# Performance work log

Measured on AMD Instinct MI355X. Metric: run time of the kernel, lower is better.

## Reference

```python
import jax, jax.numpy as jnp
import numpy as np

B, T, D, E, C = 2, 2048, 2048, 8, 512
O1 = D // E  # per-expert hidden width (out_features // num_experts)


def setup_inputs() -> dict:
    key = jax.random.key(0)
    k = jax.random.split(key, 8)
    s = 1.0 / np.sqrt(D)
    return {
        "x": jax.random.normal(k[0], (B, T, D), dtype=jnp.float32),
        "dispatch_mask": jax.random.uniform(k[1], (B, T, E, C), dtype=jnp.float32),
        "combine_array": jax.random.uniform(k[2], (B, T, E, C), dtype=jnp.float32),
        # contract weights: nn.Linear(D, D) reshaped to (E, D//E, D)
        "W1": jax.random.uniform(k[3], (E, O1, D), jnp.float32, -s, s),
        "b1": jax.random.uniform(k[4], (E, O1), jnp.float32, -s, s),
        # expand weights: nn.Linear(D, D) reshaped to (E, D, D//E)
        "W2": jax.random.uniform(k[5], (E, D, O1), jnp.float32, -s, s),
        "b2": jax.random.uniform(k[6], (D,), jnp.float32, -s, s),
    }


def reference(x, dispatch_mask, combine_array, W1, b1, W2, b2):
    # --- ExpertsChooseMaskedContract ---
    # einsum('btd,btec,eod->beco') split into two GEMM-shaped contractions
    xe = jnp.einsum('btd,btec->becd', x, dispatch_mask)          # [B,E,C,D]
    h = jnp.einsum('becd,eod->beco', xe, W1) + b1[None, :, None, :]  # [B,E,C,O1]
    # --- GELU (torch nn.GELU default = exact erf form) ---
    h = jax.nn.gelu(h, approximate=False)
    # --- ExpertsChooseMaskedExpand (homogeneous-coords bias == add b2 then combine) ---
    y = jnp.einsum('beci,eoi->beco', h, W2) + b2[None, None, None, :]  # [B,E,C,D]
    out = jnp.einsum('beco,btec->bto', y, combine_array)          # [B,T,D]
    return out
```

## Files before the change

### kernel.cpp

```cpp
#include <hip/hip_runtime.h>
#include <math.h>

#define BB 2
#define TT 2048
#define DD 2048
#define EE 8
#define CCv 512
#define OO1 256

typedef unsigned short u16;
typedef __bf16 bf16x8 __attribute__((ext_vector_type(8)));
typedef float f32x4 __attribute__((ext_vector_type(4)));

__device__ __forceinline__ u16 f2bf(float f) {
    unsigned u = __float_as_uint(f);
    unsigned r = (u + 0x7fffu + ((u >> 16) & 1u)) >> 16;
    return (u16)r;
}

__device__ __forceinline__ void gload16(const void* g, void* s) {
    __builtin_amdgcn_global_load_lds(
        (const __attribute__((address_space(1))) void*)g,
        (__attribute__((address_space(3))) void*)s, 16, 0, 0);
}

__global__ __launch_bounds__(256) void conv_cast(const float* __restrict__ in,
                                                 u16* __restrict__ out, long n) {
    long i = ((long)blockIdx.x * 256 + threadIdx.x) * 4;
    float4 v = *(const float4*)&in[i];
    ushort4 o; o.x = f2bf(v.x); o.y = f2bf(v.y); o.z = f2bf(v.z); o.w = f2bf(v.w);
    *(ushort4*)&out[i] = o;
}

__global__ __launch_bounds__(256) void dup_cast(const float* __restrict__ in,
                                                u16* __restrict__ out, long dup) {
    long i = ((long)blockIdx.x * 256 + threadIdx.x) * 4;
    float4 v = *(const float4*)&in[i];
    ushort4 o; o.x = f2bf(v.x); o.y = f2bf(v.y); o.z = f2bf(v.z); o.w = f2bf(v.w);
    *(ushort4*)&out[i] = o;
    *(ushort4*)&out[i + dup] = o;
}

__global__ __launch_bounds__(256) void gelu_fuse(const float* __restrict__ P,
                                                 const float* __restrict__ b1,
                                                 u16* __restrict__ h) {
    long i = ((long)blockIdx.x * 256 + threadIdx.x) * 4;
    const int o = (int)(i & 255);
    const int e = (int)((i >> 17) & 7);
    float4 a = *(const float4*)&P[i];
    float4 b = *(const float4*)&P[i + 4194304];
    float4 bb = *(const float4*)&b1[e * 256 + o];
    float r0 = a.x + b.x + bb.x, r1 = a.y + b.y + bb.y;
    float r2 = a.z + b.z + bb.z, r3 = a.w + b.w + bb.w;
    ushort4 o4;
    o4.x = f2bf(0.5f * r0 * (1.0f + erff(r0 * 0.70710678118654752f)));
    o4.y = f2bf(0.5f * r1 * (1.0f + erff(r1 * 0.70710678118654752f)));
    o4.z = f2bf(0.5f * r2 * (1.0f + erff(r2 * 0.70710678118654752f)));
    o4.w = f2bf(0.5f * r3 * (1.0f + erff(r3 * 0.70710678118654752f)));
    *(ushort4*)&h[i] = o4;
}

__global__ __launch_bounds__(256) void transpose_conv(
    const float* __restrict__ in, long inHi, long inLo, int modZ, long sIn,
    u16* __restrict__ out, long outZ, long sOut)
{
    __shared__ float tile[32][33];
    const int z = blockIdx.z;
    const float* ib = in + (long)(z / modZ) * inHi + (long)(z % modZ) * inLo;
    u16* ob = out + (long)z * outZ;
    const int t0 = blockIdx.y * 32, c0 = blockIdx.x * 32;
    const int tid = threadIdx.x;
    const int r = tid >> 3, c4 = (tid & 7) * 4;

    float4 v = *(const float4*)&ib[(long)(t0 + r) * sIn + c0 + c4];
    tile[r][c4 + 0] = v.x; tile[r][c4 + 1] = v.y;
    tile[r][c4 + 2] = v.z; tile[r][c4 + 3] = v.w;
    __syncthreads();

    const int oc = tid >> 3, t4 = (tid & 7) * 4;
    ushort4 o;
    o.x = f2bf(tile[t4 + 0][oc]);
    o.y = f2bf(tile[t4 + 1][oc]);
    o.z = f2bf(tile[t4 + 2][oc]);
    o.w = f2bf(tile[t4 + 3][oc]);
    *(ushort4*)&ob[(long)(c0 + oc) * sOut + t0 + t4] = o;
}

template<int EPI, int OUTBF>
__global__ __launch_bounds__(256)
void mfma_gemm(const u16* __restrict__ A, long ldA, long aHi, long aLo, int modA,
               const u16* __restrict__ B, long ldB, long bHi, long bLo, int modB,
               void* __restrict__ Cout, long ldC, long cHi, long cLo, int modC,
               const float* __restrict__ bias, long biasLo, int modBias,
               int M, int N, int K)
{
    __shared__ __align__(16) char smem[32768];
    char* smA = smem;
    char* smB = smem + 16384;

    const int z = blockIdx.z;
    const char* Ab = (const char*)(A + (long)(z / modA) * aHi + (long)(z % modA) * aLo);
    const char* Bb = (const char*)(B + (long)(z / modB) * bHi + (long)(z % modB) * bLo);
    const long ldAb = ldA * 2, ldBb = ldB * 2;

    const int m0 = blockIdx.y * 128, n0 = blockIdx.x * 128;
    const int tid = threadIdx.x;
    const int l = tid & 63;
    const int w = tid >> 6;
    const int wm = w >> 1, wn = w & 1;

    const int srow = l >> 3;
    const int schunk = (l & 7) ^ srow;
    const int frow = l & 15;
    const int fgrp = l >> 4;
    const int fch0 = fgrp ^ (l & 7);

    int aoff[4], boff[4];
#pragma unroll
    for (int i = 0; i < 4; ++i) {
        aoff[i] = (wm * 64 + i * 16 + frow) * 128 + fch0 * 16;
        boff[i] = (wn * 64 + i * 16 + frow) * 128 + fch0 * 16;
    }

    f32x4 acc[4][4];
    const f32x4 zero4 = {0.f, 0.f, 0.f, 0.f};
#pragma unroll
    for (int i = 0; i < 4; ++i)
#pragma unroll
        for (int j = 0; j < 4; ++j) acc[i][j] = zero4;

    const long sgo = (long)schunk * 16;

    for (int k0 = 0; k0 < K; k0 += 64) {
        const long kb = (long)k0 * 2;
#pragma unroll
        for (int j = 0; j < 4; ++j) {
            const int rr = (j * 4 + w) * 8 + srow;
            gload16(Ab + (long)(m0 + rr) * ldAb + kb + sgo, smA + (j * 4 + w) * 1024);
            gload16(Bb + (long)(n0 + rr) * ldBb + kb + sgo, smB + (j * 4 + w) * 1024);
        }
        __syncthreads();
#pragma unroll
        for (int kk = 0; kk < 2; ++kk) {
            const int kx = kk * 64;
            bf16x8 af[4], bfr[4];
#pragma unroll
            for (int i = 0; i < 4; ++i) af[i] = *(const bf16x8*)(smA + (aoff[i] ^ kx));
#pragma unroll
            for (int i = 0; i < 4; ++i) bfr[i] = *(const bf16x8*)(smB + (boff[i] ^ kx));
#pragma unroll
            for (int mi = 0; mi < 4; ++mi)
#pragma unroll
                for (int ni = 0; ni < 4; ++ni)
                    acc[mi][ni] = __builtin_amdgcn_mfma_f32_16x16x32_bf16(
                        af[mi], bfr[ni], acc[mi][ni], 0, 0, 0);
        }
        __syncthreads();
    }

    const long cbase = (long)(z / modC) * cHi + (long)(z % modC) * cLo;
    const float* biasB = (EPI != 0) ? (bias + (long)(z % modBias) * biasLo) : nullptr;
#pragma unroll
    for (int mi = 0; mi < 4; ++mi) {
#pragma unroll
        for (int ni = 0; ni < 4; ++ni) {
            const int col = n0 + wn * 64 + ni * 16 + frow;
            const int rowb = m0 + wm * 64 + mi * 16 + fgrp * 4;
#pragma unroll
            for (int r = 0; r < 4; ++r) {
                float v = acc[mi][ni][r];
                const int row = rowb + r;
                if (EPI == 3) v += biasB[row];
                const long idx = cbase + (long)row * ldC + col;
                if (OUTBF) ((u16*)Cout)[idx] = f2bf(v);
                else       ((float*)Cout)[idx] = v;
            }
        }
    }
}

template<int OUTBF>
__global__ __launch_bounds__(512, 2)
void mfma_gemm_256(const u16* __restrict__ A, long ldA, long aHi, long aLo, int modA,
                   const u16* __restrict__ B, long ldB, long bHi, long bLo, int modB,
                   void* __restrict__ Cout, long ldC, long cHi, long cLo, int modC,
                   int M, int N, int K)
{
    __shared__ __align__(16) char smem[131072];

    const int z = blockIdx.z;
    const char* Ab = (const char*)(A + (long)(z / modA) * aHi + (long)(z % modA) * aLo);
    const char* Bb = (const char*)(B + (long)(z / modB) * bHi + (long)(z % modB) * bLo);
    const long ldAb = ldA * 2, ldBb = ldB * 2;

    const int m0 = blockIdx.y * 256, n0 = blockIdx.x * 256;
    const int tid = threadIdx.x;
    const int l = tid & 63;
    const int w = tid >> 6;
    const int wm = w >> 2, wn = w & 3;

    const int srow = l >> 3;
    const int schunk = (l & 7) ^ srow;
    const long sgo = (long)schunk * 16;
    const int frow = l & 15, fgrp = l >> 4;
    const int cs0 = (fgrp ^ (l & 7)) * 16;

    auto stage = [&](int kt, int bsel, int half, int j) {
        const int rr = (w * 2 + j) * 8 + srow;
        const char* gb = (half < 2) ? Ab : Bb;
        const long ld = (half < 2) ? ldAb : ldBb;
        const int gr = ((half < 2) ? m0 + half * 128 : n0 + (half - 2) * 128) + rr;
        gload16(gb + (long)gr * ld + (long)kt * 128 + sgo,
                smem + bsel * 65536 + half * 16384 + (w * 2 + j) * 1024);
    };

    f32x4 acc[2][4][2][2];
    const f32x4 zero4 = {0.f, 0.f, 0.f, 0.f};
#pragma unroll
    for (int qm = 0; qm < 2; ++qm)
#pragma unroll
        for (int mi = 0; mi < 4; ++mi)
#pragma unroll
            for (int qn = 0; qn < 2; ++qn)
#pragma unroll
                for (int ni = 0; ni < 2; ++ni) acc[qm][mi][qn][ni] = zero4;

    int aoff[4], boff[2];
#pragma unroll
    for (int mi = 0; mi < 4; ++mi) aoff[mi] = (wm * 64 + mi * 16 + frow) * 128 + cs0;
#pragma unroll
    for (int ni = 0; ni < 2; ++ni) boff[ni] = (wn * 32 + ni * 16 + frow) * 128 + cs0;

    stage(0, 0, 0, 0); stage(0, 0, 0, 1);
    stage(0, 0, 2, 0); stage(0, 0, 2, 1);
    stage(0, 0, 3, 0); stage(0, 0, 3, 1);
    stage(0, 0, 1, 0); stage(0, 0, 1, 1);
    asm volatile("s_waitcnt vmcnt(4)" ::: "memory");
    __builtin_amdgcn_s_barrier();

    const int NT = K >> 6;
    for (int kt = 0; kt < NT; ++kt) {
        const char* buf = smem + (kt & 1) * 65536;
        const int sb = (kt & 1) ^ 1;
        const bool pf = (kt + 1) < NT;
        const int kn = kt + 1;
        bf16x8 af[4][2], bq0[2][2], bq1[2][2];

#pragma unroll
        for (int mi = 0; mi < 4; ++mi) {
            af[mi][0] = *(const bf16x8*)(buf + aoff[mi]);
            af[mi][1] = *(const bf16x8*)(buf + (aoff[mi] ^ 64));
        }
#pragma unroll
        for (int ni = 0; ni < 2; ++ni) {
            bq0[ni][0] = *(const bf16x8*)(buf + 32768 + boff[ni]);
            bq0[ni][1] = *(const bf16x8*)(buf + 32768 + (boff[ni] ^ 64));
        }
        if (pf) { stage(kn, sb, 0, 0); stage(kn, sb, 0, 1); }
        if (pf) { asm volatile("s_waitcnt vmcnt(4)" ::: "memory"); }
        else    { asm volatile("s_waitcnt vmcnt(2)" ::: "memory"); }
        __builtin_amdgcn_s_barrier();
        __builtin_amdgcn_s_setprio(1);
#pragma unroll
        for (int kk = 0; kk < 2; ++kk)
#pragma unroll
            for (int mi = 0; mi < 4; ++mi)
#pragma unroll
                for (int ni = 0; ni < 2; ++ni)
                    acc[0][mi][0][ni] = __builtin_amdgcn_mfma_f32_16x16x32_bf16(
                        af[mi][kk], bq0[ni][kk], acc[0][mi][0][ni], 0, 0, 0);
        __builtin_amdgcn_s_setprio(0);

#pragma unroll
        for (int ni = 0; ni < 2; ++ni) {
            bq1[ni][0] = *(const bf16x8*)(buf + 49152 + boff[ni]);
            bq1[ni][1] = *(const bf16x8*)(buf + 49152 + (boff[ni] ^ 64));
        }
        if (pf) { stage(kn, sb, 2, 0); stage(kn, sb, 2, 1); }
        if (pf) { asm volatile("s_waitcnt vmcnt(4)" ::: "memory"); }
        else    { asm volatile("s_waitcnt vmcnt(0)" ::: "memory"); }
        __builtin_amdgcn_s_barrier();
        __builtin_amdgcn_s_setprio(1);
#pragma unroll
        for (int kk = 0; kk < 2; ++kk)
#pragma unroll
            for (int mi = 0; mi < 4; ++mi)
#pragma unroll
                for (int ni = 0; ni < 2; ++ni)
                    acc[0][mi][1][ni] = __builtin_amdgcn_mfma_f32_16x16x32_bf16(
                        af[mi][kk], bq1[ni][kk], acc[0][mi][1][ni], 0, 0, 0);
        __builtin_amdgcn_s_setprio(0);

#pragma unroll
        for (int mi = 0; mi < 4; ++mi) {
            af[mi][0] = *(const bf16x8*)(buf + 16384 + aoff[mi]);
            af[mi][1] = *(const bf16x8*)(buf + 16384 + (aoff[mi] ^ 64));
        }
        if (pf) { stage(kn, sb, 3, 0); stage(kn, sb, 3, 1); }
        __builtin_amdgcn_s_setprio(1);
#pragma unroll
        for (int kk = 0; kk < 2; ++kk)
#pragma unroll
            for (int mi = 0; mi < 4; ++mi)
#pragma unroll
                for (int ni = 0; ni < 2; ++ni)
                    acc[1][mi][1][ni] = __builtin_amdgcn_mfma_f32_16x16x32_bf16(
                        af[mi][kk], bq1[ni][kk], acc[1][mi][1][ni], 0, 0, 0);
        __builtin_amdgcn_s_setprio(0);

        if (pf) { stage(kn, sb, 1, 0); stage(kn, sb, 1, 1); }
        if (pf) { asm volatile("s_waitcnt vmcnt(4)" ::: "memory"); }
        __builtin_amdgcn_s_barrier();
        __builtin_amdgcn_s_setprio(1);
#pragma unroll
        for (int kk = 0; kk < 2; ++kk)
#pragma unroll
            for (int mi = 0; mi < 4; ++mi)
#pragma unroll
                for (int ni = 0; ni < 2; ++ni)
                    acc[1][mi][0][ni] = __builtin_amdgcn_mfma_f32_16x16x32_bf16(
                        af[mi][kk], bq0[ni][kk], acc[1][mi][0][ni], 0, 0, 0);
        __builtin_amdgcn_s_setprio(0);
    }

    const long cbase = (long)(z / modC) * cHi + (long)(z % modC) * cLo;
#pragma unroll
    for (int qm = 0; qm < 2; ++qm)
#pragma unroll
        for (int mi = 0; mi < 4; ++mi)
#pragma unroll
            for (int qn = 0; qn < 2; ++qn)
#pragma unroll
                for (int ni = 0; ni < 2; ++ni) {
                    const int col = n0 + qn * 128 + wn * 32 + ni * 16 + frow;
                    const int rowb = m0 + qm * 128 + wm * 64 + mi * 16 + fgrp * 4;
#pragma unroll
                    for (int r = 0; r < 4; ++r) {
                        const float v = acc[qm][mi][qn][ni][r];
                        const long idx = cbase + (long)(rowb + r) * ldC + col;
                        if (OUTBF) ((u16*)Cout)[idx] = f2bf(v);
                        else       ((float*)Cout)[idx] = v;
                    }
                }
}

template<int EPI, int OUTBF>
__global__ __launch_bounds__(512, 2)
void mfma_gemm_big(const u16* __restrict__ A, long ldA, long aHi, long aLo, int modA,
                   const u16* __restrict__ B, long ldB, long bHi, long bLo, int modB,
                   void* __restrict__ Cout, long ldC, long cHi, long cLo, int modC,
                   const float* __restrict__ bias,
                   int M, int N, int K)
{
    __shared__ __align__(16) char smem[147456];

    const int z = blockIdx.z;
    const char* Ab = (const char*)(A + (long)(z / modA) * aHi + (long)(z % modA) * aLo);
    const char* Bb = (const char*)(B + (long)(z / modB) * bHi + (long)(z % modB) * bLo);
    const long ldAb = ldA * 2, ldBb = ldB * 2;

    const int m0 = blockIdx.y * 256, n0 = blockIdx.x * 128;
    const int tid = threadIdx.x;
    const int l = tid & 63;
    const int w = tid >> 6;
    const int wm = w >> 1, wn = w & 1;

    const int srow = l >> 3;
    const int schunk = (l & 7) ^ srow;
    const long sgo = (long)schunk * 16;
    const int frow = l & 15;
    const int fgrp = l >> 4;
    const int fsw = (fgrp ^ (l & 7)) * 16;

    auto stageA = [&](int kt, int bsel, int j) {
        const int rr = (j * 8 + w) * 8 + srow;
        gload16(Ab + (long)(m0 + rr) * ldAb + (long)kt * 128 + sgo,
                smem + bsel * 49152 + (j * 8 + w) * 1024);
    };
    auto stageB = [&](int kt, int bsel, int j) {
        const int rr = (j * 8 + w) * 8 + srow;
        gload16(Bb + (long)(n0 + rr) * ldBb + (long)kt * 128 + sgo,
                smem + bsel * 49152 + 32768 + (j * 8 + w) * 1024);
    };

    f32x4 acc[4][4];
    const f32x4 zero4 = {0.f, 0.f, 0.f, 0.f};
#pragma unroll
    for (int i = 0; i < 4; ++i)
#pragma unroll
        for (int j = 0; j < 4; ++j) acc[i][j] = zero4;

    int aoff[4], boff[4];
#pragma unroll
    for (int i = 0; i < 4; ++i) {
        aoff[i] = (wm * 64 + i * 16 + frow) * 128 + fsw;
        boff[i] = (wn * 64 + i * 16 + frow) * 128 + fsw;
    }

#pragma unroll
    for (int j = 0; j < 4; ++j) stageA(0, 0, j);
#pragma unroll
    for (int j = 0; j < 2; ++j) stageB(0, 0, j);
#pragma unroll
    for (int j = 0; j < 4; ++j) stageA(1, 1, j);
#pragma unroll
    for (int j = 0; j < 2; ++j) stageB(1, 1, j);
    asm volatile("s_waitcnt vmcnt(6)" ::: "memory");
    __builtin_amdgcn_s_barrier();

    const int NT = K >> 6;
    int bc = 0;
    int sc = 2;
    for (int kt = 0; kt < NT; ++kt) {
        const char* bufA = smem + bc * 49152;
        const char* bufB = bufA + 32768;
        const bool pf = (kt + 2) < NT;
        const int kpf = kt + 2;

        if (pf) {
            stageA(kpf, sc, 0); stageA(kpf, sc, 1);
            stageA(kpf, sc, 2); stageA(kpf, sc, 3);
            stageB(kpf, sc, 0); stageB(kpf, sc, 1);
        }

        bf16x8 af[4][2], bfr[4][2];
#pragma unroll
        for (int mi = 0; mi < 4; ++mi) {
            af[mi][0] = *(const bf16x8*)(bufA + aoff[mi]);
            af[mi][1] = *(const bf16x8*)(bufA + (aoff[mi] ^ 64));
        }
#pragma unroll
        for (int ni = 0; ni < 4; ++ni) {
            bfr[ni][0] = *(const bf16x8*)(bufB + boff[ni]);
            bfr[ni][1] = *(const bf16x8*)(bufB + (boff[ni] ^ 64));
        }

        __builtin_amdgcn_s_setprio(1);
#pragma unroll
        for (int kk = 0; kk < 2; ++kk)
#pragma unroll
            for (int mi = 0; mi < 4; ++mi)
#pragma unroll
                for (int ni = 0; ni < 4; ++ni)
                    acc[mi][ni] = __builtin_amdgcn_mfma_f32_16x16x32_bf16(
                        af[mi][kk], bfr[ni][kk], acc[mi][ni], 0, 0, 0);
        __builtin_amdgcn_s_setprio(0);

        if (pf) { asm volatile("s_waitcnt vmcnt(6)" ::: "memory"); }
        else    { asm volatile("s_waitcnt vmcnt(0)" ::: "memory"); }
        __builtin_amdgcn_s_barrier();

        bc = (bc == 2) ? 0 : bc + 1;
        sc = (sc == 2) ? 0 : sc + 1;
    }

    const long cbase = (long)(z / modC) * cHi + (long)(z % modC) * cLo;
#pragma unroll
    for (int mi = 0; mi < 4; ++mi) {
#pragma unroll
        for (int ni = 0; ni < 4; ++ni) {
            const int col = n0 + wn * 64 + ni * 16 + frow;
            const int rowb = m0 + wm * 64 + mi * 16 + fgrp * 4;
#pragma unroll
            for (int r = 0; r < 4; ++r) {
                float v = acc[mi][ni][r];
                if (EPI == 3) v += bias[rowb + r];
                const long idx = cbase + (long)(rowb + r) * ldC + col;
                if (OUTBF) ((u16*)Cout)[idx] = f2bf(v);
                else       ((float*)Cout)[idx] = v;
            }
        }
    }
}

extern "C" void kernel_launch(void* const* d_in, const int* in_sizes, int n_in,
                              void* d_out, int out_size, void* d_ws, size_t ws_size,
                              hipStream_t stream) {
    const float* x    = (const float*)d_in[0];
    const float* mask = (const float*)d_in[1];
    const float* comb = (const float*)d_in[2];
    const float* W1   = (const float*)d_in[3];
    const float* b1   = (const float*)d_in[4];
    const float* W2   = (const float*)d_in[5];
    const float* b2   = (const float*)d_in[6];
    float* out = (float*)d_out;

    char* ws = (char*)d_ws;
    u16* buf0 = (u16*)ws;
    u16* xT   = (u16*)(ws + 33554432);
    u16* W1b2 = (u16*)(ws + 33554432);
    u16* W2b  = (u16*)(ws + 58720256);
    u16* xe   = (u16*)(ws + 67108864);
    u16* h    = (u16*)(ws + 100663296);
    u16* yT   = xe;
    float* P  = (float*)ws;

    transpose_conv<<<dim3(DD / 32, TT / 32, BB), 256, 0, stream>>>(
        x, (long)TT * DD, 0L, 1, (long)DD, xT, (long)DD * TT, (long)TT);
    transpose_conv<<<dim3(CCv / 32, TT / 32, BB * EE), 256, 0, stream>>>(
        mask, (long)TT * EE * CCv, (long)CCv, EE, (long)EE * CCv,
        buf0, (long)CCv * TT, (long)TT);
    conv_cast<<<(int)((8L * DD * OO1) / 1024), 256, 0, stream>>>(W2, W2b, 8L * DD * OO1);

    mfma_gemm_256<1><<<dim3(DD / 256, CCv / 256, 16), 512, 0, stream>>>(
        buf0, 2048, 1048576L, 0L, 1,
        xT,   2048, 4194304L, 0L, 8,
        xe,   2048, 1048576L, 0L, 1,
        CCv, DD, TT);

    dup_cast<<<4096, 256, 0, stream>>>(W1, W1b2, 4194304L);

    mfma_gemm<0, 0><<<dim3(OO1 / 128, CCv / 128, 32), 256, 0, stream>>>(
        xe,   2048, 1048576L, 1024L, 2,
        W1b2, 2048, 524288L, 1024L, 2,
        P,    256, 131072L, 4194304L, 2,
        nullptr, 0L, 1, CCv, OO1, 1024);

    gelu_fuse<<<2048, 256, 0, stream>>>(P, b1, h);

    mfma_gemm<3, 1><<<dim3(CCv / 128, DD / 128, 16), 256, 0, stream>>>(
        W2b, 256, 0L, 524288L, 8,
        h,   256, 131072L, 0L, 1,
        yT,  4096, 8388608L, 512L, 8,
        b2, 0L, 1, DD, CCv, OO1);

    conv_cast<<<(int)((2L * TT * EE * CCv) / 1024), 256, 0, stream>>>(
        comb, buf0, 2L * TT * EE * CCv);

    mfma_gemm_big<0, 0><<<dim3(DD / 128, TT / 256, BB), 512, 0, stream>>>(
        buf0, 4096, 8388608L, 0L, 1,
        yT,   4096, 8388608L, 0L, 1,
        out,  2048, 4194304L, 0L, 1,
        nullptr, TT, DD, EE * CCv);
}
```

Measured before the change: 252.3 us.

## Fuse fp32-to-bf16 cast of combine array into final GEMM A-operand loading

Removes the separate conv_cast pass over the combine array. The final combine GEMM now loads fp32 A tiles into registers, converts them to bf16 and writes them swizzled into LDS, while B still streams through direct global-to-LDS loads. The aim is to avoid one full write and re-read of the 64MB-sized bf16 copy. In exchange the kernel reads fp32 A (twice the bytes per tile, read repeatedly across the N blocks), uses more registers (launch bounds drop to 1 block per CU), and its pipelining relies on hand-counted vmcnt waits.

```diff
diff --git a/kernel.cpp b/kernel.cpp
--- a/kernel.cpp
+++ b/kernel.cpp
@@ -344,20 +344,19 @@
                 }
 }
 
-template<int EPI, int OUTBF>
-__global__ __launch_bounds__(512, 2)
-void mfma_gemm_big(const u16* __restrict__ A, long ldA, long aHi, long aLo, int modA,
-                   const u16* __restrict__ B, long ldB, long bHi, long bLo, int modB,
-                   void* __restrict__ Cout, long ldC, long cHi, long cLo, int modC,
-                   const float* __restrict__ bias,
-                   int M, int N, int K)
+__global__ __launch_bounds__(512, 1)
+void mfma_gemm_big_cf(const float* __restrict__ A, long aZ,
+                      const u16* __restrict__ B, long bZ,
+                      float* __restrict__ Cout, long cZ,
+                      int M, int N, int K)
 {
     __shared__ __align__(16) char smem[147456];
 
     const int z = blockIdx.z;
-    const char* Ab = (const char*)(A + (long)(z / modA) * aHi + (long)(z % modA) * aLo);
-    const char* Bb = (const char*)(B + (long)(z / modB) * bHi + (long)(z % modB) * bLo);
-    const long ldAb = ldA * 2, ldBb = ldB * 2;
+    const float* Ab = A + (long)z * aZ;
+    const char* Bb = (const char*)(B + (long)z * bZ);
+    const long ldA = 4096;
+    const long ldBb = 4096 * 2;
 
     const int m0 = blockIdx.y * 256, n0 = blockIdx.x * 128;
     const int tid = threadIdx.x;
@@ -368,19 +367,35 @@
     const int srow = l >> 3;
     const int schunk = (l & 7) ^ srow;
     const long sgo = (long)schunk * 16;
+    const int arj = l >> 4;
+    const int ac16 = l & 15;
+    const int g = (l & 15) >> 1;
+    const int h2 = l & 1;
     const int frow = l & 15;
     const int fgrp = l >> 4;
     const int fsw = (fgrp ^ (l & 7)) * 16;
 
-    auto stageA = [&](int kt, int bsel, int j) {
-        const int rr = (j * 8 + w) * 8 + srow;
-        gload16(Ab + (long)(m0 + rr) * ldAb + (long)kt * 128 + sgo,
-                smem + bsel * 49152 + (j * 8 + w) * 1024);
-    };
-    auto stageB = [&](int kt, int bsel, int j) {
+    auto stageB = [&](int kt, int j) {
         const int rr = (j * 8 + w) * 8 + srow;
         gload16(Bb + (long)(n0 + rr) * ldBb + (long)kt * 128 + sgo,
-                smem + bsel * 49152 + 32768 + (j * 8 + w) * 1024);
+                smem + (kt % 3) * 49152 + 32768 + (j * 8 + w) * 1024);
+    };
+    auto aissue = [&](int kt, float4 (&AR)[8]) {
+#pragma unroll
+        for (int j = 0; j < 8; ++j)
+            AR[j] = *(const float4*)(Ab + (long)(m0 + w * 32 + j * 4 + arj) * ldA +
+                                     (long)kt * 64 + ac16 * 4);
+    };
+    auto aconv = [&](int kt, float4 (&AR)[8]) {
+        char* d = smem + (kt % 3) * 49152;
+#pragma unroll
+        for (int j = 0; j < 8; ++j) {
+            const int r = w * 32 + j * 4 + arj;
+            ushort4 o;
+            o.x = f2bf(AR[j].x); o.y = f2bf(AR[j].y);
+            o.z = f2bf(AR[j].z); o.w = f2bf(AR[j].w);
+            *(ushort4*)(d + r * 128 + ((g ^ (r & 7)) * 16) + h2 * 8) = o;
+        }
     };
 
     f32x4 acc[4][4];
@@ -397,64 +412,65 @@
         boff[i] = (wn * 64 + i * 16 + frow) * 128 + fsw;
     }
 
-#pragma unroll
-    for (int j = 0; j < 4; ++j) stageA(0, 0, j);
-#pragma unroll
-    for (int j = 0; j < 2; ++j) stageB(0, 0, j);
-#pragma unroll
-    for (int j = 0; j < 4; ++j) stageA(1, 1, j);
-#pragma unroll
-    for (int j = 0; j < 2; ++j) stageB(1, 1, j);
-    asm volatile("s_waitcnt vmcnt(6)" ::: "memory");
+    float4 aR0[8], aR1[8];
+    aissue(0, aR0);
+    stageB(0, 0); stageB(0, 1);
+    aissue(1, aR1);
+    stageB(1, 0); stageB(1, 1);
+    asm volatile("s_waitcnt vmcnt(12)" ::: "memory");
+    aconv(0, aR0);
+    asm volatile("s_waitcnt vmcnt(10)" ::: "memory");
+    asm volatile("s_waitcnt lgkmcnt(0)" ::: "memory");
     __builtin_amdgcn_s_barrier();
 
     const int NT = K >> 6;
-    int bc = 0;
-    int sc = 2;
-    for (int kt = 0; kt < NT; ++kt) {
-        const char* bufA = smem + bc * 49152;
-        const char* bufB = bufA + 32768;
-        const bool pf = (kt + 2) < NT;
-        const int kpf = kt + 2;
-
-        if (pf) {
-            stageA(kpf, sc, 0); stageA(kpf, sc, 1);
-            stageA(kpf, sc, 2); stageA(kpf, sc, 3);
-            stageB(kpf, sc, 0); stageB(kpf, sc, 1);
-        }
-
-        bf16x8 af[4][2], bfr[4][2];
-#pragma unroll
-        for (int mi = 0; mi < 4; ++mi) {
-            af[mi][0] = *(const bf16x8*)(bufA + aoff[mi]);
-            af[mi][1] = *(const bf16x8*)(bufA + (aoff[mi] ^ 64));
-        }
-#pragma unroll
-        for (int ni = 0; ni < 4; ++ni) {
-            bfr[ni][0] = *(const bf16x8*)(bufB + boff[ni]);
-            bfr[ni][1] = *(const bf16x8*)(bufB + (boff[ni] ^ 64));
-        }
-
-        __builtin_amdgcn_s_setprio(1);
-#pragma unroll
-        for (int kk = 0; kk < 2; ++kk)
-#pragma unroll
-            for (int mi = 0; mi < 4; ++mi)
-#pragma unroll
-                for (int ni = 0; ni < 4; ++ni)
-                    acc[mi][ni] = __builtin_amdgcn_mfma_f32_16x16x32_bf16(
-                        af[mi][kk], bfr[ni][kk], acc[mi][ni], 0, 0, 0);
-        __builtin_amdgcn_s_setprio(0);
-
-        if (pf) { asm volatile("s_waitcnt vmcnt(6)" ::: "memory"); }
-        else    { asm volatile("s_waitcnt vmcnt(0)" ::: "memory"); }
-        __builtin_amdgcn_s_barrier();
-
-        bc = (bc == 2) ? 0 : bc + 1;
-        sc = (sc == 2) ? 0 : sc + 1;
-    }
-
-    const long cbase = (long)(z / modC) * cHi + (long)(z % modC) * cLo;
+
+#define CF_TILE(KT, ARI, ARC)                                                   \
+    {                                                                           \
+        const int kt = (KT);                                                    \
+        const bool pf2 = (kt + 2) < NT, pf1 = (kt + 1) < NT;                    \
+        if (pf2) { aissue(kt + 2, ARI); stageB(kt + 2, 0); stageB(kt + 2, 1); } \
+        if (pf1) {                                                              \
+            if (pf2) { asm volatile("s_waitcnt vmcnt(12)" ::: "memory"); }      \
+            else     { asm volatile("s_waitcnt vmcnt(2)" ::: "memory"); }       \
+            aconv(kt + 1, ARC);                                                 \
+        }                                                                       \
+        const char* bufA = smem + (kt % 3) * 49152;                             \
+        const char* bufB = bufA + 32768;                                        \
+        bf16x8 af[4][2], bfr[4][2];                                             \
+        _Pragma("unroll")                                                       \
+        for (int mi = 0; mi < 4; ++mi) {                                        \
+            af[mi][0] = *(const bf16x8*)(bufA + aoff[mi]);                      \
+            af[mi][1] = *(const bf16x8*)(bufA + (aoff[mi] ^ 64));               \
+        }                                                                       \
+        _Pragma("unroll")                                                       \
+        for (int ni = 0; ni < 4; ++ni) {                                        \
+            bfr[ni][0] = *(const bf16x8*)(bufB + boff[ni]);                     \
+            bfr[ni][1] = *(const bf16x8*)(bufB + (boff[ni] ^ 64));              \
+        }                                                                       \
+        __builtin_amdgcn_s_setprio(1);                                          \
+        _Pragma("unroll")                                                       \
+        for (int kk = 0; kk < 2; ++kk)                                          \
+            _Pragma("unroll")                                                   \
+            for (int mi = 0; mi < 4; ++mi)                                      \
+                _Pragma("unroll")                                               \
+                for (int ni = 0; ni < 4; ++ni)                                  \
+                    acc[mi][ni] = __builtin_amdgcn_mfma_f32_16x16x32_bf16(      \
+                        af[mi][kk], bfr[ni][kk], acc[mi][ni], 0, 0, 0);         \
+        __builtin_amdgcn_s_setprio(0);                                          \
+        if (pf1 && pf2) { asm volatile("s_waitcnt vmcnt(10)" ::: "memory"); }   \
+        else            { asm volatile("s_waitcnt vmcnt(0)" ::: "memory"); }    \
+        asm volatile("s_waitcnt lgkmcnt(0)" ::: "memory");                      \
+        __builtin_amdgcn_s_barrier();                                           \
+    }
+
+    for (int it = 0; it < NT / 2; ++it) {
+        CF_TILE(2 * it,     aR0, aR1);
+        CF_TILE(2 * it + 1, aR1, aR0);
+    }
+#undef CF_TILE
+
+    const long cbase = (long)z * cZ;
 #pragma unroll
     for (int mi = 0; mi < 4; ++mi) {
 #pragma unroll
@@ -463,11 +479,7 @@
             const int rowb = m0 + wm * 64 + mi * 16 + fgrp * 4;
 #pragma unroll
             for (int r = 0; r < 4; ++r) {
-                float v = acc[mi][ni][r];
-                if (EPI == 3) v += bias[rowb + r];
-                const long idx = cbase + (long)(rowb + r) * ldC + col;
-                if (OUTBF) ((u16*)Cout)[idx] = f2bf(v);
-                else       ((float*)Cout)[idx] = v;
+                Cout[cbase + (long)(rowb + r) * 2048 + col] = acc[mi][ni][r];
             }
         }
     }
@@ -524,12 +536,9 @@
         yT,  4096, 8388608L, 512L, 8,
         b2, 0L, 1, DD, CCv, OO1);
 
-    conv_cast<<<(int)((2L * TT * EE * CCv) / 1024), 256, 0, stream>>>(
-        comb, buf0, 2L * TT * EE * CCv);
-
-    mfma_gemm_big<0, 0><<<dim3(DD / 128, TT / 256, BB), 512, 0, stream>>>(
-        buf0, 4096, 8388608L, 0L, 1,
-        yT,   4096, 8388608L, 0L, 1,
-        out,  2048, 4194304L, 0L, 1,
-        nullptr, TT, DD, EE * CCv);
-}
+    mfma_gemm_big_cf<<<dim3(DD / 128, TT / 256, BB), 512, 0, stream>>>(
+        comb, 8388608L,
+        yT,   8388608L,
+        out,  4194304L,
+        TT, DD, EE * CCv);
+}
```

New measurement: 317.7 us. 25.9% more time.
